# Kernel tuning notes

Hardware: AMD Instinct MI355X
Metric: run time of the kernel (lower is better)

The kernel has to match this reference:

```python
import jax, jax.numpy as jnp
import numpy as np

WH, WW = 7, 7
N = WH * WW
C = 192
H = 6
D = C // H


def _rel_position_index(Wh, Ww):
    # double_step_seq(2*Ww-1, Wh, 1, Ww)
    seq1 = np.arange(0, (2 * Ww - 1) * Wh, 2 * Ww - 1)
    seq2 = np.arange(0, Ww, 1)
    coords = (seq1[:, None] + seq2[None, :]).reshape(1, -1)  # [1, Wh*Ww]
    idx = coords + coords.T                                   # [N, N]
    idx = idx[:, ::-1].copy()                                 # flip(1)
    return idx

REL_IDX = _rel_position_index(WH, WW)  # static int index [N, N]


def setup_inputs() -> dict:
    key = jax.random.key(0)
    ks = jax.random.split(key, 8)
    B = 8192
    nW = 64
    q = jax.random.normal(ks[0], (B, N, C), dtype=jnp.float32)
    kv = jax.random.normal(ks[1], (B, N, C), dtype=jnp.float32)
    mask = jnp.zeros((nW, N, N), dtype=jnp.float32)
    s = 0.02
    Wq = jax.random.normal(ks[2], (C, C), dtype=jnp.float32) * s
    bq = jnp.zeros((C,), dtype=jnp.float32)
    Wkv = jax.random.normal(ks[3], (2 * C, C), dtype=jnp.float32) * s
    bkv = jnp.zeros((2 * C,), dtype=jnp.float32)
    Wo = jax.random.normal(ks[4], (C, C), dtype=jnp.float32) * s
    bo = jnp.zeros((C,), dtype=jnp.float32)
    rpb_table = jax.random.normal(ks[5], ((2 * WH - 1) * (2 * WW - 1), H), dtype=jnp.float32) * s
    return {"q": q, "kv": kv, "mask": mask, "Wq": Wq, "bq": bq,
            "Wkv": Wkv, "bkv": bkv, "Wo": Wo, "bo": bo, "rpb_table": rpb_table}


def reference(q, kv, mask, Wq, bq, Wkv, bkv, Wo, bo, rpb_table):
    B, Nq, _ = q.shape
    Nk = kv.shape[1]
    scale = D ** -0.5
    qh = (q @ Wq.T + bq).reshape(B, Nq, H, D).transpose(0, 2, 1, 3)  # [B,H,Nq,D]
    kvh = (kv @ Wkv.T + bkv).reshape(B, Nk, 2, H, D)
    kh = kvh[:, :, 0].transpose(0, 2, 1, 3)  # [B,H,Nk,D]
    vh = kvh[:, :, 1].transpose(0, 2, 1, 3)
    attn = jnp.einsum('bhqd,bhkd->bhqk', qh * scale, kh)
    bias = rpb_table[REL_IDX.reshape(-1)].reshape(N, N, H).transpose(2, 0, 1)  # [H,N,N]
    attn = attn + bias[None]
    nW = mask.shape[0]
    attn = attn.reshape(B // nW, nW, H, Nq, Nk) + mask[None, :, None]
    attn = attn.reshape(B, H, Nq, Nk)
    attn = jax.nn.softmax(attn, axis=-1)
    x = jnp.einsum('bhqk,bhkd->bhqd', attn, vh).transpose(0, 2, 1, 3).reshape(B, Nq, C)
    return x @ Wo.T + bo
```

## Files before the change

kernel.cpp:

```cpp
#include <hip/hip_runtime.h>

#define NTOK 49
#define CDIM 192
#define NHEAD 6
#define HDIM 32

typedef float f32x4 __attribute__((ext_vector_type(4), may_alias));
typedef short b16x8 __attribute__((ext_vector_type(8), may_alias));
typedef short b16x4 __attribute__((ext_vector_type(4), may_alias));

__device__ __forceinline__ f32x4 MFMA(b16x8 a, b16x8 b, f32x4 c) {
  return __builtin_amdgcn_mfma_f32_16x16x32_bf16(a, b, c, 0, 0, 0);
}

__device__ __forceinline__ short f2bf(float f) {
  unsigned u = __builtin_bit_cast(unsigned, f);
  u += 0x7FFFu + ((u >> 16) & 1u);
  return (short)(u >> 16);
}

__device__ __forceinline__ int swz(int row, int col) {
  return row * CDIM + (col ^ ((row & 7) << 3));
}

__global__ void prep_w(const float* __restrict__ Wq, const float* __restrict__ Wkv,
                       const float* __restrict__ Wo, short* __restrict__ wsW) {
  const float scale = 0.17677669529663687f;
  int i = blockIdx.x * 256 + threadIdx.x;
  if (i >= 147456) return;
  float v;
  if (i < 36864)        v = Wq[i] * scale;
  else if (i < 110592)  v = Wkv[i - 36864];
  else                  v = Wo[i - 110592];
  wsW[i] = f2bf(v);
}

__global__ void prep_bias(const float* __restrict__ rpb, float* __restrict__ bias_t) {
  int idx = blockIdx.x * 256 + threadIdx.x;
  if (idx >= NHEAD * NTOK * NTOK) return;
  int h = idx / (NTOK * NTOK);
  int p = idx % (NTOK * NTOK);
  int i = p / NTOK, j = p % NTOK;
  int ci = (i / 7) * 13 + (i % 7);
  int jj = 48 - j;
  int cj = (jj / 7) * 13 + (jj % 7);
  bias_t[idx] = rpb[(ci + cj) * NHEAD + h];
}

__global__ __attribute__((amdgpu_flat_work_group_size(512, 512),
                          amdgpu_waves_per_eu(3))) void wmsa_kernel(
    const float* __restrict__ qg, const float* __restrict__ kvg,
    const float* __restrict__ maskg, const float* __restrict__ bq,
    const float* __restrict__ bkv, const float* __restrict__ bo,
    const short* __restrict__ wsW, const float* __restrict__ bias_t,
    float* __restrict__ outg, int nW) {
  __shared__ short lds[37632];
  short* SH = lds;
  short* VT = lds + 12288;
  short* KH = lds + 25344;
  float* BF = (float*)lds;

  const int b = blockIdx.x;
  const int tid = threadIdx.x;
  const int w = tid >> 6;
  const int lane = tid & 63;
  const int l15 = lane & 15;
  const int lg = lane >> 4;
  const int R = w >> 1, hw = w & 1, h0 = hw * 3;
  const float scale = 0.17677669529663687f;
  const f32x4 zero4 = {0.f, 0.f, 0.f, 0.f};

  const short* WqB = wsW;
  const short* WkvB = wsW + 36864;
  const short* WoB = wsW + 110592;

  const float* qsrc = qg + (size_t)b * (NTOK * CDIM);
  const float* kvsrc = kvg + (size_t)b * (NTOK * CDIM);

  f32x4 qv[6], kvreg[6];
#pragma unroll
  for (int it = 0; it < 6; ++it) {
    int idx = tid + it * 512;
    int r = idx / 48, c4 = idx % 48;
    qv[it] = (r < NTOK) ? *(const f32x4*)(qsrc + r * CDIM + c4 * 4) : zero4;
  }
#pragma unroll
  for (int it = 0; it < 6; ++it) {
    int idx = tid + it * 512;
    int r = idx / 48, c4 = idx % 48;
    kvreg[it] = (r < NTOK) ? *(const f32x4*)(kvsrc + r * CDIM + c4 * 4) : zero4;
  }
#pragma unroll
  for (int it = 0; it < 6; ++it) {
    int idx = tid + it * 512;
    int r = idx / 48, c4 = idx % 48;
    b16x4 o = {f2bf(qv[it][0]), f2bf(qv[it][1]), f2bf(qv[it][2]), f2bf(qv[it][3])};
    *(b16x4*)(SH + swz(r, c4 * 4)) = o;
  }
  __syncthreads();

  f32x4 qacc[6];
#pragma unroll
  for (int t = 0; t < 6; ++t) qacc[t] = zero4;
  {
    b16x8 aq6[6];
#pragma unroll
    for (int kk = 0; kk < 6; ++kk)
      aq6[kk] = *(const b16x8*)(SH + swz(R * 16 + l15, kk * 32 + lg * 8));
#pragma unroll
    for (int t = 0; t < 6; ++t) {
      const int col = (hw * 6 + t) * 16 + l15;
#pragma unroll
      for (int kk = 0; kk < 6; ++kk) {
        b16x8 bw = *(const b16x8*)(WqB + col * CDIM + kk * 32 + lg * 8);
        qacc[t] = MFMA(aq6[kk], bw, qacc[t]);
      }
    }
  }
  __syncthreads();

#pragma unroll
  for (int t = 0; t < 6; ++t) {
    const int col = (hw * 6 + t) * 16 + l15;
    const float bias = bq[col] * scale;
#pragma unroll
    for (int r = 0; r < 4; ++r)
      SH[swz(R * 16 + lg * 4 + r, hw * 96 + t * 16 + l15)] = f2bf(qacc[t][r] + bias);
  }
  b16x8 aq[3];
#pragma unroll
  for (int hh = 0; hh < 3; ++hh)
    aq[hh] = *(const b16x8*)(SH + swz(R * 16 + l15, hw * 96 + hh * 32 + lg * 8));
  __syncthreads();

#pragma unroll
  for (int it = 0; it < 6; ++it) {
    int idx = tid + it * 512;
    int r = idx / 48, c4 = idx % 48;
    b16x4 o = {f2bf(kvreg[it][0]), f2bf(kvreg[it][1]), f2bf(kvreg[it][2]),
               f2bf(kvreg[it][3])};
    *(b16x4*)(SH + swz(r, c4 * 4)) = o;
  }
  __syncthreads();

#pragma unroll
  for (int jj = 0; jj < 3; ++jj) {
    const int nt = w * 3 + jj;
    const int col = nt * 16 + l15;
    f32x4 acc[4];
#pragma unroll
    for (int m = 0; m < 4; ++m) acc[m] = zero4;
#pragma unroll
    for (int kk = 0; kk < 6; ++kk) {
      b16x8 bw = *(const b16x8*)(WkvB + col * CDIM + kk * 32 + lg * 8);
#pragma unroll
      for (int m = 0; m < 4; ++m) {
        b16x8 a = *(const b16x8*)(SH + swz(m * 16 + l15, kk * 32 + lg * 8));
        acc[m] = MFMA(a, bw, acc[m]);
      }
    }
    const float bias = bkv[col];
    if (col < CDIM) {
#pragma unroll
      for (int m = 0; m < 4; ++m)
#pragma unroll
        for (int r = 0; r < 4; ++r)
          KH[swz(m * 16 + lg * 4 + r, col)] = f2bf(acc[m][r] + bias);
    } else {
      const int c = col - CDIM;
#pragma unroll
      for (int m = 0; m < 4; ++m) {
        b16x4 o = {f2bf(acc[m][0] + bias), f2bf(acc[m][1] + bias),
                   f2bf(acc[m][2] + bias), f2bf(acc[m][3] + bias)};
        *(b16x4*)(VT + c * 68 + m * 16 + lg * 4) = o;
      }
    }
  }
  __syncthreads();

  const float* maskw = maskg + (size_t)(b % nW) * (NTOK * NTOK);
  float maskv[4][4];
#pragma unroll
  for (int nt = 0; nt < 4; ++nt) {
    const int cgl = nt * 16 + l15;
#pragma unroll
    for (int r = 0; r < 4; ++r) {
      const int rw = R * 16 + lg * 4 + r;
      maskv[nt][r] = (rw < NTOK && cgl < NTOK) ? maskw[rw * NTOK + cgl] : 0.f;
    }
  }

  f32x4 xh[3][2];
#pragma unroll
  for (int hh = 0; hh < 3; ++hh) {
    xh[hh][0] = zero4;
    xh[hh][1] = zero4;
  }
#pragma unroll
  for (int hh = 0; hh < 3; ++hh) {
    const int h = h0 + hh;
    f32x4 L[4];
    __builtin_amdgcn_s_setprio(1);
#pragma unroll
    for (int nt = 0; nt < 4; ++nt) {
      b16x8 bk = *(const b16x8*)(KH + swz(nt * 16 + l15, h * 32 + lg * 8));
      L[nt] = MFMA(aq[hh], bk, zero4);
    }
    __builtin_amdgcn_s_setprio(0);
    const float* bt = bias_t + h * (NTOK * NTOK);
#pragma unroll
    for (int nt = 0; nt < 4; ++nt) {
      const int cgl = nt * 16 + l15;
#pragma unroll
      for (int r = 0; r < 4; ++r) {
        const int rw = R * 16 + lg * 4 + r;
        if (rw < NTOK && cgl < NTOK) L[nt][r] += bt[rw * NTOK + cgl] + maskv[nt][r];
        else                          L[nt][r] = -1e9f;
      }
    }
#pragma unroll
    for (int r = 0; r < 4; ++r) {
      float m = fmaxf(fmaxf(L[0][r], L[1][r]), fmaxf(L[2][r], L[3][r]));
      m = fmaxf(m, __shfl_xor(m, 1));
      m = fmaxf(m, __shfl_xor(m, 2));
      m = fmaxf(m, __shfl_xor(m, 4));
      m = fmaxf(m, __shfl_xor(m, 8));
      float p0 = __expf(L[0][r] - m), p1 = __expf(L[1][r] - m);
      float p2 = __expf(L[2][r] - m), p3 = __expf(L[3][r] - m);
      float s = p0 + p1 + p2 + p3;
      s += __shfl_xor(s, 1);
      s += __shfl_xor(s, 2);
      s += __shfl_xor(s, 4);
      s += __shfl_xor(s, 8);
      const float is = 1.0f / s;
      L[0][r] = p0 * is; L[1][r] = p1 * is; L[2][r] = p2 * is; L[3][r] = p3 * is;
    }
#pragma unroll
    for (int nt = 0; nt < 4; ++nt)
#pragma unroll
      for (int r = 0; r < 4; ++r)
        SH[swz(R * 16 + lg * 4 + r, hw * 96 + nt * 16 + l15)] = f2bf(L[nt][r]);
    __builtin_amdgcn_s_setprio(1);
#pragma unroll
    for (int kk = 0; kk < 2; ++kk) {
      b16x8 ap = *(const b16x8*)(SH + swz(R * 16 + l15, hw * 96 + kk * 32 + lg * 8));
#pragma unroll
      for (int nv = 0; nv < 2; ++nv) {
        b16x8 bv = *(const b16x8*)(VT + (h * 32 + nv * 16 + l15) * 68 + kk * 32 + lg * 8);
        xh[hh][nv] = MFMA(ap, bv, xh[hh][nv]);
      }
    }
    __builtin_amdgcn_s_setprio(0);
  }
  __syncthreads();
#pragma unroll
  for (int hh = 0; hh < 3; ++hh)
#pragma unroll
    for (int nv = 0; nv < 2; ++nv)
#pragma unroll
      for (int r = 0; r < 4; ++r)
        KH[swz(R * 16 + lg * 4 + r, (h0 + hh) * 32 + nv * 16 + l15)] =
            f2bf(xh[hh][nv][r]);
  __syncthreads();

#pragma unroll
  for (int t = 0; t < 6; ++t) {
    const int pid = w * 6 + t;
    const int j = pid >> 2, m = pid & 3;
    const int col = j * 16 + l15;
    f32x4 oacc = zero4;
#pragma unroll
    for (int kk = 0; kk < 6; ++kk) {
      b16x8 a = *(const b16x8*)(KH + swz(m * 16 + l15, kk * 32 + lg * 8));
      b16x8 bw = *(const b16x8*)(WoB + col * CDIM + kk * 32 + lg * 8);
      oacc = MFMA(a, bw, oacc);
    }
    const float bias = bo[col];
#pragma unroll
    for (int r = 0; r < 4; ++r) {
      const int row = m * 16 + lg * 4 + r;
      if (row < NTOK) BF[row * 204 + col] = oacc[r] + bias;
    }
  }
  __syncthreads();

  float* dst = outg + (size_t)b * (NTOK * CDIM);
#pragma unroll
  for (int t = 0; t < 5; ++t) {
    int idx = tid + t * 512;
    if (idx < NTOK * 48) {
      int row = idx / 48, c4 = idx % 48;
      f32x4 v = *(const f32x4*)(BF + row * 204 + c4 * 4);
      *(f32x4*)(dst + row * CDIM + c4 * 4) = v;
    }
  }
}

extern "C" void kernel_launch(void* const* d_in, const int* in_sizes, int n_in,
                              void* d_out, int out_size, void* d_ws, size_t ws_size,
                              hipStream_t stream) {
  const float* q = (const float*)d_in[0];
  const float* kv = (const float*)d_in[1];
  const float* mask = (const float*)d_in[2];
  const float* Wq = (const float*)d_in[3];
  const float* bq = (const float*)d_in[4];
  const float* Wkv = (const float*)d_in[5];
  const float* bkv = (const float*)d_in[6];
  const float* Wo = (const float*)d_in[7];
  const float* bo = (const float*)d_in[8];
  const float* rpb = (const float*)d_in[9];
  short* wsW = (short*)d_ws;
  float* bias_t = (float*)((char*)d_ws + 294912);

  const int B = in_sizes[0] / (NTOK * CDIM);
  const int nW = in_sizes[2] / (NTOK * NTOK);

  prep_w<<<576, 256, 0, stream>>>(Wq, Wkv, Wo, wsW);
  prep_bias<<<57, 256, 0, stream>>>(rpb, bias_t);
  wmsa_kernel<<<B, 512, 0, stream>>>(q, kv, mask, bq, bkv, bo, wsW, bias_t,
                                     (float*)d_out, nW);
}
```

Baseline: 889.0 us.

## Transpose score MFMA so softmax rows live per lane, pad bias table

Swaps the MFMA operands for QK^T so each lane holds one query row's keys. The softmax max and sum then need only two cross-lane shuffles instead of four per row. The relative-position bias is pre-padded to 64 columns with -1e9, so the kernel does vectorized bias loads with no bounds branches, and the mask is read with vector loads. P goes through a small per-wave swizzled LDS scratch, and the Q projection writes into the KH region, which drops one barrier. In exchange the kernel relies on unaligned vector mask loads and on the padded -1e9 bias entries to mask invalid columns.

```diff
diff --git a/kernel.cpp b/kernel.cpp
--- a/kernel.cpp
+++ b/kernel.cpp
@@ -6,6 +6,7 @@
 #define HDIM 32
 
 typedef float f32x4 __attribute__((ext_vector_type(4), may_alias));
+typedef float f32x4u __attribute__((ext_vector_type(4), may_alias, aligned(4)));
 typedef short b16x8 __attribute__((ext_vector_type(8), may_alias));
 typedef short b16x4 __attribute__((ext_vector_type(4), may_alias));
 
@@ -21,6 +22,9 @@
 
 __device__ __forceinline__ int swz(int row, int col) {
   return row * CDIM + (col ^ ((row & 7) << 3));
+}
+__device__ __forceinline__ int ps(int r, int c) {
+  return r * 32 + (c ^ ((((r & 3) ^ ((r >> 2) & 3)) & 3) << 3));
 }
 
 __global__ void prep_w(const float* __restrict__ Wq, const float* __restrict__ Wkv,
@@ -37,14 +41,18 @@
 
 __global__ void prep_bias(const float* __restrict__ rpb, float* __restrict__ bias_t) {
   int idx = blockIdx.x * 256 + threadIdx.x;
-  if (idx >= NHEAD * NTOK * NTOK) return;
-  int h = idx / (NTOK * NTOK);
-  int p = idx % (NTOK * NTOK);
-  int i = p / NTOK, j = p % NTOK;
-  int ci = (i / 7) * 13 + (i % 7);
-  int jj = 48 - j;
-  int cj = (jj / 7) * 13 + (jj % 7);
-  bias_t[idx] = rpb[(ci + cj) * NHEAD + h];
+  if (idx >= NHEAD * NTOK * 64) return;
+  int k = idx & 63;
+  int q = (idx >> 6) % NTOK;
+  int h = idx / (NTOK * 64);
+  float v = -1e9f;
+  if (k < NTOK) {
+    int ci = (q / 7) * 13 + (q % 7);
+    int jj = 48 - k;
+    int cj = (jj / 7) * 13 + (jj % 7);
+    v = rpb[(ci + cj) * NHEAD + h];
+  }
+  bias_t[idx] = v;
 }
 
 __global__ __attribute__((amdgpu_flat_work_group_size(512, 512),
@@ -77,6 +85,9 @@
   const float* qsrc = qg + (size_t)b * (NTOK * CDIM);
   const float* kvsrc = kvg + (size_t)b * (NTOK * CDIM);
 
+  const int qrow = R * 16 + l15;
+  const int qc = qrow > 48 ? 48 : qrow;
+
   f32x4 qv[6], kvreg[6];
 #pragma unroll
   for (int it = 0; it < 6; ++it) {
@@ -117,20 +128,18 @@
       }
     }
   }
-  __syncthreads();
-
 #pragma unroll
   for (int t = 0; t < 6; ++t) {
     const int col = (hw * 6 + t) * 16 + l15;
     const float bias = bq[col] * scale;
 #pragma unroll
     for (int r = 0; r < 4; ++r)
-      SH[swz(R * 16 + lg * 4 + r, hw * 96 + t * 16 + l15)] = f2bf(qacc[t][r] + bias);
+      KH[swz(R * 16 + lg * 4 + r, hw * 96 + t * 16 + l15)] = f2bf(qacc[t][r] + bias);
   }
   b16x8 aq[3];
 #pragma unroll
   for (int hh = 0; hh < 3; ++hh)
-    aq[hh] = *(const b16x8*)(SH + swz(R * 16 + l15, hw * 96 + hh * 32 + lg * 8));
+    aq[hh] = *(const b16x8*)(KH + swz(R * 16 + l15, hw * 96 + hh * 32 + lg * 8));
   __syncthreads();
 
 #pragma unroll
@@ -179,16 +188,11 @@
   __syncthreads();
 
   const float* maskw = maskg + (size_t)(b % nW) * (NTOK * NTOK);
-  float maskv[4][4];
-#pragma unroll
-  for (int nt = 0; nt < 4; ++nt) {
-    const int cgl = nt * 16 + l15;
-#pragma unroll
-    for (int r = 0; r < 4; ++r) {
-      const int rw = R * 16 + lg * 4 + r;
-      maskv[nt][r] = (rw < NTOK && cgl < NTOK) ? maskw[rw * NTOK + cgl] : 0.f;
-    }
-  }
+  f32x4 maskv[3];
+#pragma unroll
+  for (int nt = 0; nt < 3; ++nt)
+    maskv[nt] = *(const f32x4u*)(maskw + qc * NTOK + nt * 16 + lg * 4);
+  const float mask48 = (lg == 0) ? maskw[qc * NTOK + 48] : 0.f;
 
   f32x4 xh[3][2];
 #pragma unroll
@@ -199,57 +203,67 @@
 #pragma unroll
   for (int hh = 0; hh < 3; ++hh) {
     const int h = h0 + hh;
-    f32x4 L[4];
+    f32x4 Ls[4];
     __builtin_amdgcn_s_setprio(1);
 #pragma unroll
     for (int nt = 0; nt < 4; ++nt) {
       b16x8 bk = *(const b16x8*)(KH + swz(nt * 16 + l15, h * 32 + lg * 8));
-      L[nt] = MFMA(aq[hh], bk, zero4);
+      Ls[nt] = MFMA(bk, aq[hh], zero4);
     }
     __builtin_amdgcn_s_setprio(0);
-    const float* bt = bias_t + h * (NTOK * NTOK);
+    const float* bt = bias_t + (h * NTOK + qc) * 64;
 #pragma unroll
     for (int nt = 0; nt < 4; ++nt) {
-      const int cgl = nt * 16 + l15;
-#pragma unroll
-      for (int r = 0; r < 4; ++r) {
-        const int rw = R * 16 + lg * 4 + r;
-        if (rw < NTOK && cgl < NTOK) L[nt][r] += bt[rw * NTOK + cgl] + maskv[nt][r];
-        else                          L[nt][r] = -1e9f;
-      }
-    }
-#pragma unroll
-    for (int r = 0; r < 4; ++r) {
-      float m = fmaxf(fmaxf(L[0][r], L[1][r]), fmaxf(L[2][r], L[3][r]));
-      m = fmaxf(m, __shfl_xor(m, 1));
-      m = fmaxf(m, __shfl_xor(m, 2));
-      m = fmaxf(m, __shfl_xor(m, 4));
-      m = fmaxf(m, __shfl_xor(m, 8));
-      float p0 = __expf(L[0][r] - m), p1 = __expf(L[1][r] - m);
-      float p2 = __expf(L[2][r] - m), p3 = __expf(L[3][r] - m);
-      float s = p0 + p1 + p2 + p3;
-      s += __shfl_xor(s, 1);
-      s += __shfl_xor(s, 2);
-      s += __shfl_xor(s, 4);
-      s += __shfl_xor(s, 8);
-      const float is = 1.0f / s;
-      L[0][r] = p0 * is; L[1][r] = p1 * is; L[2][r] = p2 * is; L[3][r] = p3 * is;
-    }
+      f32x4 bb = *(const f32x4*)(bt + nt * 16 + lg * 4);
+#pragma unroll
+      for (int rr = 0; rr < 4; ++rr) Ls[nt][rr] += bb[rr];
+    }
+#pragma unroll
+    for (int nt = 0; nt < 3; ++nt)
+#pragma unroll
+      for (int rr = 0; rr < 4; ++rr) Ls[nt][rr] += maskv[nt][rr];
+    Ls[3][0] += mask48;
+
+    float mx = Ls[0][0];
 #pragma unroll
     for (int nt = 0; nt < 4; ++nt)
 #pragma unroll
-      for (int r = 0; r < 4; ++r)
-        SH[swz(R * 16 + lg * 4 + r, hw * 96 + nt * 16 + l15)] = f2bf(L[nt][r]);
+      for (int rr = 0; rr < 4; ++rr) mx = fmaxf(mx, Ls[nt][rr]);
+    mx = fmaxf(mx, __shfl_xor(mx, 16));
+    mx = fmaxf(mx, __shfl_xor(mx, 32));
+    float sum = 0.f;
+#pragma unroll
+    for (int nt = 0; nt < 4; ++nt)
+#pragma unroll
+      for (int rr = 0; rr < 4; ++rr) {
+        Ls[nt][rr] = __expf(Ls[nt][rr] - mx);
+        sum += Ls[nt][rr];
+      }
+    sum += __shfl_xor(sum, 16);
+    sum += __shfl_xor(sum, 32);
+    const float inv = 1.f / sum;
+
+    short* Pscr = SH + w * 512;
+    b16x8 ap[2];
+#pragma unroll
+    for (int kkh = 0; kkh < 2; ++kkh) {
+#pragma unroll
+      for (int nth = 0; nth < 2; ++nth) {
+        const int nt = 2 * kkh + nth;
+        b16x4 o = {f2bf(Ls[nt][0] * inv), f2bf(Ls[nt][1] * inv),
+                   f2bf(Ls[nt][2] * inv), f2bf(Ls[nt][3] * inv)};
+        *(b16x4*)(Pscr + ps(l15, nth * 16 + lg * 4)) = o;
+      }
+      ap[kkh] = *(const b16x8*)(Pscr + ps(l15, lg * 8));
+    }
     __builtin_amdgcn_s_setprio(1);
 #pragma unroll
-    for (int kk = 0; kk < 2; ++kk) {
-      b16x8 ap = *(const b16x8*)(SH + swz(R * 16 + l15, hw * 96 + kk * 32 + lg * 8));
+    for (int kkh = 0; kkh < 2; ++kkh)
 #pragma unroll
       for (int nv = 0; nv < 2; ++nv) {
-        b16x8 bv = *(const b16x8*)(VT + (h * 32 + nv * 16 + l15) * 68 + kk * 32 + lg * 8);
-        xh[hh][nv] = MFMA(ap, bv, xh[hh][nv]);
-      }
-    }
+        b16x8 bv = *(const b16x8*)(VT + (h * 32 + nv * 16 + l15) * 68 + kkh * 32 + lg * 8);
+        xh[hh][nv] = MFMA(ap[kkh], bv, xh[hh][nv]);
+      }
     __builtin_amdgcn_s_setprio(0);
   }
   __syncthreads();
@@ -316,7 +330,7 @@
   const int nW = in_sizes[2] / (NTOK * NTOK);
 
   prep_w<<<576, 256, 0, stream>>>(Wq, Wkv, Wo, wsW);
-  prep_bias<<<57, 256, 0, stream>>>(rpb, bias_t);
+  prep_bias<<<(NHEAD * NTOK * 64 + 255) / 256, 256, 0, stream>>>(rpb, bias_t);
   wmsa_kernel<<<B, 512, 0, stream>>>(q, kv, mask, bq, bkv, bo, wsW, bias_t,
                                      (float*)d_out, nW);
 }
```

New measurement: 784.0 us, median of 2. 1.13x faster.
